# Kernel optimization log

Measured on AMD Instinct MI355X. Metric: run time of the kernel, lower is better.

Reference implementation:

```python
import jax, jax.numpy as jnp
import numpy as np
import math

B, T, D, H = 128, 512, 512, 512


def setup_inputs() -> dict:
    key = jax.random.key(0)
    ks = jax.random.split(key, 6)
    s = 1.0 / math.sqrt(H)
    return {
        "values": jax.random.normal(ks[0], (B, T, D), jnp.float32),
        "Deltas": jax.random.uniform(ks[1], (B, T, D), jnp.float32),
        "W_att": jax.random.normal(ks[2], (D, D), jnp.float32) * s,
        "b_att": jnp.zeros((D,), jnp.float32),
        "W_ih": jax.random.normal(ks[3], (4 * H, D), jnp.float32) * s,
        "W_hh": jax.random.normal(ks[4], (4 * H, H), jnp.float32) * s,
        "b_ih": jnp.zeros((4 * H,), jnp.float32),
        "b_hh": jnp.zeros((4 * H,), jnp.float32),
    }


def lstm_cell(x, h, c, W_ih, W_hh, b_ih, b_hh):
    # torch.nn.LSTMCell: gates ordered i, f, g, o
    g = x @ W_ih.T + b_ih + h @ W_hh.T + b_hh
    i, f, gg, o = jnp.split(g, 4, axis=-1)
    c2 = jax.nn.sigmoid(f) * c + jax.nn.sigmoid(i) * jnp.tanh(gg)
    h2 = jax.nn.sigmoid(o) * jnp.tanh(c2)
    return h2, c2


def reference(values, Deltas, W_att, b_att, W_ih, W_hh, b_ih, b_hh):
    Bn, Tn, Dn = values.shape
    Hn = W_hh.shape[1]
    # cumsum over time then reverse along time (reverse_tensor)
    Del = jnp.flip(jnp.cumsum(Deltas, axis=-2), axis=1)  # [B,T,D]
    v_att = values @ W_att.T + b_att                      # attn-projected inputs [B,T,D]
    # a_ij = bmm(atten_linear(values), values^T) -> [B,T,T]
    a_ij = jnp.einsum('btd,bsd->bts', v_att, values)
    h0 = jnp.zeros((Bn, Hn), values.dtype)
    c0 = jnp.zeros((Bn, Hn), values.dtype)

    def step(carry, x_t):
        h, c = carry
        h2, c2 = lstm_cell(x_t, h, c, W_ih, W_hh, b_ih, b_hh)
        return (h2, c2), (h2, c2)

    xs = jnp.swapaxes(v_att[:, :-1], 0, 1)  # [T-1, B, D]
    (h_last, _), (hs, cs) = jax.lax.scan(step, (h0, c0), xs)
    hs = jnp.swapaxes(hs, 0, 1)  # [B, T-1, H]
    cs = jnp.swapaxes(cs, 0, 1)  # [B, T-1, H]

    # attention-weighted cell-state mixing for the final step
    alpha = jax.nn.softmax(a_ij[:, -1, :-1], axis=-1)[..., None]  # [B,T-1,1]
    d = Del[:, 1:]                                                # [B,T-1,D]
    C_i = jnp.sum(alpha * cs / jnp.log(math.e + d), axis=1)       # [B,H]

    hT, cT = lstm_cell(v_att[:, -1], h_last, C_i, W_ih, W_hh, b_ih, b_hh)
    h_n = jnp.concatenate([hs, hT[:, None, :]], axis=1)  # [B,T,H]
    return h_n
```

## Files before the change

kernel.cpp:

```cpp
#include <hip/hip_runtime.h>
#include <cstdint>

#define DEVI __device__ __forceinline__

typedef unsigned short ushort_t;
typedef __attribute__((ext_vector_type(8))) short s16x8;
typedef __attribute__((ext_vector_type(4))) int i32x4;
typedef __attribute__((ext_vector_type(4))) float f32x4;

DEVI ushort_t f2bf(float f) {
  uint32_t u = __builtin_bit_cast(uint32_t, f);
  u += 0x7fffu + ((u >> 16) & 1u);
  return (ushort_t)(u >> 16);
}
DEVI float bf2f(ushort_t u) {
  uint32_t x = ((uint32_t)u) << 16;
  return __builtin_bit_cast(float, x);
}
DEVI float sigmoidf_(float x) { return 1.0f / (1.0f + __expf(-x)); }
DEVI float tanhf_(float x) {
  float e = __expf(-2.0f * fabsf(x));
  float r = (1.0f - e) / (1.0f + e);
  return copysignf(r, x);
}

DEVI void load_mallx4(i32x4& dst, const uint32_t* p) {
  asm volatile("global_load_dwordx4 %0, %1, off sc0 sc1" : "=v"(dst) : "v"(p));
}
DEVI void store_mall(uint32_t* p, uint32_t v) {
  asm volatile("global_store_dword %0, %1, off sc0 sc1" :: "v"(p), "v"(v) : "memory");
}
DEVI void wait_vm0() { asm volatile("s_waitcnt vmcnt(0)" ::: "memory"); }

__global__ void cast_kernel(const float* __restrict__ in, ushort_t* __restrict__ out, long n) {
  long i = ((long)blockIdx.x * blockDim.x + threadIdx.x) * 8;
  if (i >= n) return;
  float4 a = *(const float4*)(in + i);
  float4 b = *(const float4*)(in + i + 4);
  union { s16x8 v; ushort_t u[8]; } r;
  r.u[0] = f2bf(a.x); r.u[1] = f2bf(a.y); r.u[2] = f2bf(a.z); r.u[3] = f2bf(a.w);
  r.u[4] = f2bf(b.x); r.u[5] = f2bf(b.y); r.u[6] = f2bf(b.z); r.u[7] = f2bf(b.w);
  *(s16x8*)(out + i) = r.v;
}

__global__ void transpose512(const float* __restrict__ in, float* __restrict__ out) {
  __shared__ float tile[32][33];
  int bx = blockIdx.x * 32, by = blockIdx.y * 32;
  int tx = threadIdx.x, ty = threadIdx.y;
  for (int i = 0; i < 32; i += 8)
    tile[ty + i][tx] = in[(by + ty + i) * 512 + bx + tx];
  __syncthreads();
  for (int i = 0; i < 32; i += 8)
    out[(bx + ty + i) * 512 + by + tx] = tile[tx][ty + i];
}

__global__ __launch_bounds__(256, 2)
void gemm_bt(const ushort_t* __restrict__ A, const ushort_t* __restrict__ B,
             const float* __restrict__ bias0, const float* __restrict__ bias1,
             ushort_t* __restrict__ C, int N, int K) {
  __shared__ __align__(16) ushort_t As[128 * 64];
  __shared__ __align__(16) ushort_t Bs[128 * 64];
  const int tid = threadIdx.x;
  const int lane = tid & 63, wv = tid >> 6;
  const int wm = wv >> 1, wn = wv & 1;
  const int l15 = lane & 15, l4 = lane >> 4;
  const long m0 = (long)blockIdx.x * 128;
  const int n0 = blockIdx.y * 128;
  const int nkt = K / 64;

  f32x4 acc[4][4] = {};

  int soff[4];
#pragma unroll
  for (int i = 0; i < 4; ++i) {
    int c = tid + i * 256;
    int r = c >> 3, ks = c & 7;
    soff[i] = r * 64 + ((ks ^ (r & 7)) << 3);
  }

#pragma unroll
  for (int i = 0; i < 4; ++i) {
    int c = tid + i * 256; int r = c >> 3; int ks = c & 7;
    *(s16x8*)&As[soff[i]] = *(const s16x8*)&A[(m0 + r) * K + ks * 8];
    *(s16x8*)&Bs[soff[i]] = *(const s16x8*)&B[(long)(n0 + r) * K + ks * 8];
  }
  __syncthreads();

  for (int kt = 0; kt < nkt; ++kt) {
    s16x8 ra[4], rb[4];
    const bool more = (kt + 1 < nkt);
    if (more) {
      const long kb = (long)(kt + 1) * 64;
#pragma unroll
      for (int i = 0; i < 4; ++i) {
        int c = tid + i * 256; int r = c >> 3; int ks = c & 7;
        ra[i] = *(const s16x8*)&A[(m0 + r) * K + kb + ks * 8];
        rb[i] = *(const s16x8*)&B[(long)(n0 + r) * K + kb + ks * 8];
      }
    }
#pragma unroll
    for (int kk = 0; kk < 2; ++kk) {
      s16x8 af[4], bfv[4];
      int slot = kk * 4 + l4;
#pragma unroll
      for (int i = 0; i < 4; ++i) {
        int rA = wm * 64 + i * 16 + l15;
        af[i] = *(const s16x8*)&As[rA * 64 + ((slot ^ (rA & 7)) << 3)];
        int rB = wn * 64 + i * 16 + l15;
        bfv[i] = *(const s16x8*)&Bs[rB * 64 + ((slot ^ (rB & 7)) << 3)];
      }
#pragma unroll
      for (int i = 0; i < 4; ++i)
#pragma unroll
        for (int j = 0; j < 4; ++j)
          acc[i][j] = __builtin_amdgcn_mfma_f32_16x16x32_bf16(af[i], bfv[j], acc[i][j], 0, 0, 0);
    }
    __syncthreads();
    if (more) {
#pragma unroll
      for (int i = 0; i < 4; ++i) {
        *(s16x8*)&As[soff[i]] = ra[i];
        *(s16x8*)&Bs[soff[i]] = rb[i];
      }
      __syncthreads();
    }
  }
#pragma unroll
  for (int i = 0; i < 4; ++i) {
#pragma unroll
    for (int j = 0; j < 4; ++j) {
#pragma unroll
      for (int r = 0; r < 4; ++r) {
        long m = m0 + wm * 64 + i * 16 + l4 * 4 + r;
        int n = n0 + wn * 64 + j * 16 + l15;
        float v = acc[i][j][r];
        if (bias0) v += bias0[n];
        if (bias1) v += bias1[n];
        C[m * (long)N + n] = f2bf(v);
      }
    }
  }
}

__global__ void bias_combo_kernel(const float* __restrict__ W_ih, const float* __restrict__ b_att,
                                  const float* __restrict__ b_ih, const float* __restrict__ b_hh,
                                  float* __restrict__ bc) {
  int n = blockIdx.x * 256 + threadIdx.x;
  __shared__ float ba[512];
  for (int k = threadIdx.x; k < 512; k += 256) ba[k] = b_att[k];
  __syncthreads();
  float s = b_ih[n] + b_hh[n];
  const float* row = W_ih + (long)n * 512;
  for (int k = 0; k < 512; ++k) s += row[k] * ba[k];
  bc[n] = s;
}

__global__ void vT_kernel(const float* __restrict__ values, const float* __restrict__ W_attT,
                          const float* __restrict__ b_att, float* __restrict__ vT) {
  int b = blockIdx.y;
  int n = blockIdx.x * 256 + threadIdx.x;
  __shared__ float xr[512];
  const float* row = values + ((long)b * 512 + 511) * 512;
  for (int k = threadIdx.x; k < 512; k += 256) xr[k] = row[k];
  __syncthreads();
  float acc = b_att[n];
  for (int k = 0; k < 512; ++k) acc += xr[k] * W_attT[k * 512 + n];
  vT[b * 512 + n] = acc;
}

__global__ void dtot_kernel(const float* __restrict__ Deltas, float* __restrict__ Dtot) {
  int idx = blockIdx.x * 256 + threadIdx.x;
  int b = idx >> 9, ch = idx & 511;
  const float* p = Deltas + (long)b * 512 * 512 + ch;
  float s = 0.0f;
  for (int t = 0; t < 511; ++t) s += p[(long)t * 512];
  Dtot[idx] = s;
}

__global__ void logits_kernel(const float* __restrict__ values, const float* __restrict__ vT,
                              float* __restrict__ logits) {
  int b = blockIdx.y;
  int wave = threadIdx.x >> 6, lane = threadIdx.x & 63;
  float vreg[8];
  const float* vtb = vT + b * 512;
#pragma unroll
  for (int j = 0; j < 8; ++j) vreg[j] = vtb[lane * 8 + j];
  int s0 = blockIdx.x * 64 + wave * 16;
  for (int si = 0; si < 16; ++si) {
    int s = s0 + si;
    if (s >= 511) break;
    const float* row = values + ((long)b * 512 + s) * 512 + lane * 8;
    float4 a = *(const float4*)row;
    float4 c = *(const float4*)(row + 4);
    float d = a.x * vreg[0] + a.y * vreg[1] + a.z * vreg[2] + a.w * vreg[3] +
              c.x * vreg[4] + c.y * vreg[5] + c.z * vreg[6] + c.w * vreg[7];
#pragma unroll
    for (int off = 32; off; off >>= 1) d += __shfl_xor(d, off);
    if (lane == 0) logits[b * 512 + s] = d;
  }
}

__global__ void softmax_kernel(float* __restrict__ logits) {
  int b = blockIdx.x, tid = threadIdx.x;
  __shared__ float wmax[4], wsum[4];
  float v0 = (tid < 511) ? logits[b * 512 + tid] : -1e30f;
  float v1 = (tid + 256 < 511) ? logits[b * 512 + tid + 256] : -1e30f;
  float m = fmaxf(v0, v1);
#pragma unroll
  for (int off = 32; off; off >>= 1) m = fmaxf(m, __shfl_xor(m, off));
  if ((tid & 63) == 0) wmax[tid >> 6] = m;
  __syncthreads();
  m = fmaxf(fmaxf(wmax[0], wmax[1]), fmaxf(wmax[2], wmax[3]));
  float e0 = (tid < 511) ? __expf(v0 - m) : 0.0f;
  float e1 = (tid + 256 < 511) ? __expf(v1 - m) : 0.0f;
  float s = e0 + e1;
#pragma unroll
  for (int off = 32; off; off >>= 1) s += __shfl_xor(s, off);
  if ((tid & 63) == 0) wsum[tid >> 6] = s;
  __syncthreads();
  s = wsum[0] + wsum[1] + wsum[2] + wsum[3];
  float inv = 1.0f / s;
  __syncthreads();
  if (tid < 511) logits[b * 512 + tid] = e0 * inv;
  if (tid + 256 < 511) logits[b * 512 + tid + 256] = e1 * inv;
}

__global__ __launch_bounds__(512, 1)
void scan_kernel(const float* __restrict__ W_hh, const ushort_t* __restrict__ Gx,
                 const float* __restrict__ alpha, const float* __restrict__ Dtot,
                 const float* __restrict__ Deltas, uint32_t* __restrict__ hbuf32,
                 float* __restrict__ out) {
  __shared__ __align__(16) ushort_t whh[128 * 512];
  float* gbufF = (float*)whh;
  const int tid = threadIdx.x;
  const int bg = blockIdx.x & 7, hc = blockIdx.x >> 3;
  const int b0 = bg * 16, n0 = hc * 32;
  const int lane = tid & 63, wv = tid >> 6;
  const int ks = wv & 3, hcol = wv >> 2;
  const int l15 = lane & 15, l4 = lane >> 4;
  const int eb = tid >> 5, eh = tid & 31;
  const int bglob = b0 + eb, hglob = n0 + eh;

  for (int idx = tid; idx < 128 * 512; idx += 512) {
    int r = idx >> 9, k = idx & 511;
    int grow = (r >> 5) * 512 + n0 + ((r >> 4) & 1) * 16 + (r & 15);
    float v = W_hh[(long)grow * 512 + k];
    int off = r * 512 + ((((k >> 3) ^ (r & 7)) << 3) | (k & 7));
    whh[off] = f2bf(v);
  }
  float c_state = 0.0f, Cacc = 0.0f;
  float running = Dtot[bglob * 512 + hglob];
  __syncthreads();

  s16x8 bfr[4][4];
#pragma unroll
  for (int g = 0; g < 4; ++g) {
    const int brow = g * 32 + hcol * 16 + l15;
#pragma unroll
    for (int kk4 = 0; kk4 < 4; ++kk4) {
      int k = ks * 128 + kk4 * 32 + l4 * 8;
      int slot = (k >> 3) ^ (brow & 7);
      bfr[g][kk4] = *(const s16x8*)&whh[brow * 512 + (slot << 3)];
    }
  }
  __syncthreads();

  const uint32_t pollOff = (uint32_t)(l15 * 512 + ks * 128 + l4 * 8);
  const uint32_t wOff = (uint32_t)(eb * 512 + hglob);
  uint32_t* slab[2] = { hbuf32 + bg * 8192, hbuf32 + (8 + bg) * 8192 };
  const ushort_t* gxbase = Gx + (long)bglob * 512 * 2048 + hglob;
  const float* dbase = Deltas + (long)bglob * 512 * 512 + hglob;
  const float* abase = alpha + bglob * 512;
  float* obase = out + (long)bglob * 512 * 512 + hglob;

  auto GIDX = [](int h2, int k4, int g, int row, int col) {
    return (((h2 * 4 + k4) * 4 + g) * 16 + row) * 18 + col;
  };

  for (int t = 0; t < 512; ++t) {
    float a_t = 0.0f, delta_t = 0.0f;
    if (t < 511) {
      a_t = abase[t];
      delta_t = dbase[(long)(510 - t) * 512];
    }
    ushort_t gxr[4];
#pragma unroll
    for (int g = 0; g < 4; ++g)
      gxr[g] = gxbase[(long)t * 2048 + g * 512];
    float rl = 1.0f / __logf(2.71828182845904523f + running);

    const uint32_t* pb = slab[t & 1] + pollOff;
    const uint32_t expect = (uint32_t)t << 16;
    i32x4 q[8];
    int sweeps = 0;
    for (;;) {
#pragma unroll
      for (int k = 0; k < 4; ++k) {
        load_mallx4(q[k * 2], pb + k * 32);
        load_mallx4(q[k * 2 + 1], pb + k * 32 + 4);
      }
      wait_vm0();
      __builtin_amdgcn_sched_barrier(0);
      uint32_t bad = 0;
#pragma unroll
      for (int i = 0; i < 8; ++i) {
        bad |= (uint32_t)q[i][0] ^ expect;
        bad |= (uint32_t)q[i][1] ^ expect;
        bad |= (uint32_t)q[i][2] ^ expect;
        bad |= (uint32_t)q[i][3] ^ expect;
      }
      if (!__any((bad & 0xffff0000u) != 0)) break;
      if (++sweeps > (1 << 15)) break;
      if (sweeps > 2) {
        __builtin_amdgcn_s_sleep(4);
      } else {
        __builtin_amdgcn_s_sleep(1);
      }
    }
    s16x8 afr[4];
#pragma unroll
    for (int kk4 = 0; kk4 < 4; ++kk4) {
      union { uint32_t d[4]; s16x8 v; } u;
      u.d[0] = __builtin_amdgcn_perm((uint32_t)q[kk4 * 2][1], (uint32_t)q[kk4 * 2][0], 0x05040100u);
      u.d[1] = __builtin_amdgcn_perm((uint32_t)q[kk4 * 2][3], (uint32_t)q[kk4 * 2][2], 0x05040100u);
      u.d[2] = __builtin_amdgcn_perm((uint32_t)q[kk4 * 2 + 1][1], (uint32_t)q[kk4 * 2 + 1][0], 0x05040100u);
      u.d[3] = __builtin_amdgcn_perm((uint32_t)q[kk4 * 2 + 1][3], (uint32_t)q[kk4 * 2 + 1][2], 0x05040100u);
      afr[kk4] = u.v;
    }
    f32x4 acc[4] = {};
#pragma unroll
    for (int kk4 = 0; kk4 < 4; ++kk4)
#pragma unroll
      for (int g = 0; g < 4; ++g)
        acc[g] = __builtin_amdgcn_mfma_f32_16x16x32_bf16(afr[kk4], bfr[g][kk4], acc[g], 0, 0, 0);

#pragma unroll
    for (int g = 0; g < 4; ++g)
#pragma unroll
      for (int r = 0; r < 4; ++r)
        gbufF[GIDX(hcol, ks, g, l4 * 4 + r, l15)] = acc[g][r];
    __syncthreads();

    const int hr = eh >> 4, col = eh & 15;
    float gate[4];
#pragma unroll
    for (int g = 0; g < 4; ++g)
      gate[g] = gbufF[GIDX(hr, 0, g, eb, col)] + gbufF[GIDX(hr, 1, g, eb, col)] +
                gbufF[GIDX(hr, 2, g, eb, col)] + gbufF[GIDX(hr, 3, g, eb, col)] + bf2f(gxr[g]);
    __syncthreads();

    float cin = (t == 511) ? Cacc : c_state;
    float cnew = sigmoidf_(gate[1]) * cin + sigmoidf_(gate[0]) * tanhf_(gate[2]);
    float hnew = sigmoidf_(gate[3]) * tanhf_(cnew);

    if (t < 511) {
      uint32_t w = ((uint32_t)(t + 1) << 16) | (uint32_t)f2bf(hnew);
      store_mall(slab[(t + 1) & 1] + wOff, w);
      obase[(long)t * 512] = hnew;
      c_state = cnew;
      Cacc += a_t * cnew * rl;
      running -= delta_t;
    } else {
      obase[(long)t * 512] = hnew;
    }
  }
}

extern "C" void kernel_launch(void* const* d_in, const int* in_sizes, int n_in,
                              void* d_out, int out_size, void* d_ws, size_t ws_size,
                              hipStream_t stream) {
  const float* values = (const float*)d_in[0];
  const float* Deltas = (const float*)d_in[1];
  const float* W_att  = (const float*)d_in[2];
  const float* b_att  = (const float*)d_in[3];
  const float* W_ih   = (const float*)d_in[4];
  const float* W_hh   = (const float*)d_in[5];
  const float* b_ih   = (const float*)d_in[6];
  const float* b_hh   = (const float*)d_in[7];
  float* out = (float*)d_out;

  char* ws = (char*)d_ws;
  size_t off = 0;
  auto alloc = [&](size_t bytes) -> void* {
    void* p = ws + off;
    off += (bytes + 255) & ~(size_t)255;
    return p;
  };
  ushort_t* values_bf = (ushort_t*)alloc(67108864ull);
  ushort_t* Gx        = (ushort_t*)alloc(268435456ull);
  ushort_t* W_ih_bf   = (ushort_t*)alloc(2097152ull);
  ushort_t* Wc_bf     = (ushort_t*)alloc(2097152ull);
  float*    W_attT    = (float*)alloc(1048576ull);
  ushort_t* W_attT_bf = (ushort_t*)alloc(524288ull);
  float*    vT        = (float*)alloc(262144ull);
  float*    Dtot      = (float*)alloc(262144ull);
  float*    alpha     = (float*)alloc(262144ull);
  float*    bias_c    = (float*)alloc(8192ull);
  uint32_t* hbuf32    = (uint32_t*)alloc(524288ull);

  (void)hipMemsetAsync(hbuf32, 0, 524288ull, stream);

  cast_kernel<<<33554432 / 8 / 256, 256, 0, stream>>>(values, values_bf, 33554432L);
  cast_kernel<<<1048576 / 8 / 256, 256, 0, stream>>>(W_ih, W_ih_bf, 1048576L);
  transpose512<<<dim3(16, 16), dim3(32, 8), 0, stream>>>(W_att, W_attT);
  cast_kernel<<<262144 / 8 / 256, 256, 0, stream>>>(W_attT, W_attT_bf, 262144L);

  gemm_bt<<<dim3(16, 4), 256, 0, stream>>>(W_ih_bf, W_attT_bf, nullptr, nullptr,
                                           Wc_bf, 512, 512);
  bias_combo_kernel<<<8, 256, 0, stream>>>(W_ih, b_att, b_ih, b_hh, bias_c);

  gemm_bt<<<dim3(512, 16), 256, 0, stream>>>(values_bf, Wc_bf, bias_c, nullptr,
                                             Gx, 2048, 512);

  vT_kernel<<<dim3(2, 128), 256, 0, stream>>>(values, W_attT, b_att, vT);
  dtot_kernel<<<256, 256, 0, stream>>>(Deltas, Dtot);
  logits_kernel<<<dim3(8, 128), 256, 0, stream>>>(values, vT, alpha);
  softmax_kernel<<<128, 256, 0, stream>>>(alpha);

  scan_kernel<<<128, 512, 0, stream>>>(W_hh, Gx, alpha, Dtot, Deltas, hbuf32, out);
}
```

Before: 2.715 ms.

## Split LSTM scan across 256 blocks with per-step atomic counter barrier

Halves the hidden-column slice per block (16 instead of 32) and launches 256 blocks of 256 threads, so each wave handles a full k-slice and the W_hh tile in LDS shrinks. Adds a per-batch-group global counter that each wave increments after publishing its h values; consumers spin on the counter before polling the tagged h slab. Double-buffers the gate reduction buffer in LDS to drop one __syncthreads per step. This spreads the recurrent work over more CUs but adds cross-block synchronization traffic (atomics plus waits) on every timestep.

```diff
diff --git a/kernel.cpp b/kernel.cpp
--- a/kernel.cpp
+++ b/kernel.cpp
@@ -26,6 +26,12 @@
 
 DEVI void load_mallx4(i32x4& dst, const uint32_t* p) {
   asm volatile("global_load_dwordx4 %0, %1, off sc0 sc1" : "=v"(dst) : "v"(p));
+}
+DEVI int load_cnt(const int* p) {
+  int r;
+  asm volatile("global_load_dword %0, %1, off sc0 sc1\n\ts_waitcnt vmcnt(0)"
+               : "=v"(r) : "v"(p) : "memory");
+  return r;
 }
 DEVI void store_mall(uint32_t* p, uint32_t v) {
   asm volatile("global_store_dword %0, %1, off sc0 sc1" :: "v"(p), "v"(v) : "memory");
@@ -225,25 +231,24 @@
   if (tid + 256 < 511) logits[b * 512 + tid + 256] = e1 * inv;
 }
 
-__global__ __launch_bounds__(512, 1)
+__global__ __launch_bounds__(256, 1)
 void scan_kernel(const float* __restrict__ W_hh, const ushort_t* __restrict__ Gx,
                  const float* __restrict__ alpha, const float* __restrict__ Dtot,
                  const float* __restrict__ Deltas, uint32_t* __restrict__ hbuf32,
-                 float* __restrict__ out) {
-  __shared__ __align__(16) ushort_t whh[128 * 512];
-  float* gbufF = (float*)whh;
+                 int* __restrict__ cnt, float* __restrict__ out) {
+  __shared__ __align__(16) ushort_t whh[64 * 512];
+  __shared__ float gbuf[2][4][4][16][20];
   const int tid = threadIdx.x;
   const int bg = blockIdx.x & 7, hc = blockIdx.x >> 3;
-  const int b0 = bg * 16, n0 = hc * 32;
+  const int b0 = bg * 16, n0 = hc * 16;
   const int lane = tid & 63, wv = tid >> 6;
-  const int ks = wv & 3, hcol = wv >> 2;
   const int l15 = lane & 15, l4 = lane >> 4;
-  const int eb = tid >> 5, eh = tid & 31;
+  const int eb = tid >> 4, eh = tid & 15;
   const int bglob = b0 + eb, hglob = n0 + eh;
 
-  for (int idx = tid; idx < 128 * 512; idx += 512) {
+  for (int idx = tid; idx < 64 * 512; idx += 256) {
     int r = idx >> 9, k = idx & 511;
-    int grow = (r >> 5) * 512 + n0 + ((r >> 4) & 1) * 16 + (r & 15);
+    int grow = (r >> 4) * 512 + n0 + (r & 15);
     float v = W_hh[(long)grow * 512 + k];
     int off = r * 512 + ((((k >> 3) ^ (r & 7)) << 3) | (k & 7));
     whh[off] = f2bf(v);
@@ -255,27 +260,23 @@
   s16x8 bfr[4][4];
 #pragma unroll
   for (int g = 0; g < 4; ++g) {
-    const int brow = g * 32 + hcol * 16 + l15;
+    const int brow = g * 16 + l15;
 #pragma unroll
     for (int kk4 = 0; kk4 < 4; ++kk4) {
-      int k = ks * 128 + kk4 * 32 + l4 * 8;
+      int k = wv * 128 + kk4 * 32 + l4 * 8;
       int slot = (k >> 3) ^ (brow & 7);
       bfr[g][kk4] = *(const s16x8*)&whh[brow * 512 + (slot << 3)];
     }
   }
-  __syncthreads();
-
-  const uint32_t pollOff = (uint32_t)(l15 * 512 + ks * 128 + l4 * 8);
+
+  const uint32_t pollOff = (uint32_t)(l15 * 512 + wv * 128 + l4 * 8);
   const uint32_t wOff = (uint32_t)(eb * 512 + hglob);
   uint32_t* slab[2] = { hbuf32 + bg * 8192, hbuf32 + (8 + bg) * 8192 };
+  int* cntbg = cnt + bg * 512;
   const ushort_t* gxbase = Gx + (long)bglob * 512 * 2048 + hglob;
   const float* dbase = Deltas + (long)bglob * 512 * 512 + hglob;
   const float* abase = alpha + bglob * 512;
   float* obase = out + (long)bglob * 512 * 512 + hglob;
-
-  auto GIDX = [](int h2, int k4, int g, int row, int col) {
-    return (((h2 * 4 + k4) * 4 + g) * 16 + row) * 18 + col;
-  };
 
   for (int t = 0; t < 512; ++t) {
     float a_t = 0.0f, delta_t = 0.0f;
@@ -289,6 +290,16 @@
       gxr[g] = gxbase[(long)t * 2048 + g * 512];
     float rl = 1.0f / __logf(2.71828182845904523f + running);
 
+    if (t > 0) {
+      const int* cp = cntbg + (t - 1);
+      int guard = 0;
+      for (;;) {
+        if (load_cnt(cp) >= 128) break;
+        if (++guard > (1 << 17)) break;
+        __builtin_amdgcn_s_sleep(1);
+      }
+    }
+
     const uint32_t* pb = slab[t & 1] + pollOff;
     const uint32_t expect = (uint32_t)t << 16;
     i32x4 q[8];
@@ -311,11 +322,7 @@
       }
       if (!__any((bad & 0xffff0000u) != 0)) break;
       if (++sweeps > (1 << 15)) break;
-      if (sweeps > 2) {
-        __builtin_amdgcn_s_sleep(4);
-      } else {
-        __builtin_amdgcn_s_sleep(1);
-      }
+      __builtin_amdgcn_s_sleep(1);
     }
     s16x8 afr[4];
 #pragma unroll
@@ -334,20 +341,19 @@
       for (int g = 0; g < 4; ++g)
         acc[g] = __builtin_amdgcn_mfma_f32_16x16x32_bf16(afr[kk4], bfr[g][kk4], acc[g], 0, 0, 0);
 
+    const int p = t & 1;
 #pragma unroll
     for (int g = 0; g < 4; ++g)
 #pragma unroll
       for (int r = 0; r < 4; ++r)
-        gbufF[GIDX(hcol, ks, g, l4 * 4 + r, l15)] = acc[g][r];
+        gbuf[p][wv][g][l4 * 4 + r][l15] = acc[g][r];
     __syncthreads();
 
-    const int hr = eh >> 4, col = eh & 15;
     float gate[4];
 #pragma unroll
     for (int g = 0; g < 4; ++g)
-      gate[g] = gbufF[GIDX(hr, 0, g, eb, col)] + gbufF[GIDX(hr, 1, g, eb, col)] +
-                gbufF[GIDX(hr, 2, g, eb, col)] + gbufF[GIDX(hr, 3, g, eb, col)] + bf2f(gxr[g]);
-    __syncthreads();
+      gate[g] = gbuf[p][0][g][eb][eh] + gbuf[p][1][g][eb][eh] +
+                gbuf[p][2][g][eb][eh] + gbuf[p][3][g][eb][eh] + bf2f(gxr[g]);
 
     float cin = (t == 511) ? Cacc : c_state;
     float cnew = sigmoidf_(gate[1]) * cin + sigmoidf_(gate[0]) * tanhf_(gate[2]);
@@ -356,6 +362,9 @@
     if (t < 511) {
       uint32_t w = ((uint32_t)(t + 1) << 16) | (uint32_t)f2bf(hnew);
       store_mall(slab[(t + 1) & 1] + wOff, w);
+      wait_vm0();
+      if (lane == 0)
+        __hip_atomic_fetch_add(cntbg + t, 1, __ATOMIC_RELAXED, __HIP_MEMORY_SCOPE_AGENT);
       obase[(long)t * 512] = hnew;
       c_state = cnew;
       Cacc += a_t * cnew * rl;
@@ -397,8 +406,9 @@
   float*    alpha     = (float*)alloc(262144ull);
   float*    bias_c    = (float*)alloc(8192ull);
   uint32_t* hbuf32    = (uint32_t*)alloc(524288ull);
-
-  (void)hipMemsetAsync(hbuf32, 0, 524288ull, stream);
+  int*      cnt       = (int*)alloc(16384ull);
+
+  (void)hipMemsetAsync(hbuf32, 0, 524288ull + 16384ull, stream);
 
   cast_kernel<<<33554432 / 8 / 256, 256, 0, stream>>>(values, values_bf, 33554432L);
   cast_kernel<<<1048576 / 8 / 256, 256, 0, stream>>>(W_ih, W_ih_bf, 1048576L);
@@ -417,5 +427,5 @@
   logits_kernel<<<dim3(8, 128), 256, 0, stream>>>(values, vT, alpha);
   softmax_kernel<<<128, 256, 0, stream>>>(alpha);
 
-  scan_kernel<<<128, 512, 0, stream>>>(W_hh, Gx, alpha, Dtot, Deltas, hbuf32, out);
-}
+  scan_kernel<<<256, 256, 0, stream>>>(W_hh, Gx, alpha, Dtot, Deltas, hbuf32, cnt, out);
+}
```

After: 2.503 ms. 1.09x faster.
